# Performance work log

Measured on AMD Instinct MI355X. Metric: run time of the kernel, lower is better.

## Reference

```python
import jax, jax.numpy as jnp
import numpy as np

FP8_MAX = 448.0   # max normal of float8_e4m3fn
BLOCK = 128       # block_size
EPS = 1e-12


def setup_inputs() -> dict:
    key = jax.random.key(0)
    k1, k2 = jax.random.split(key)
    M, K, N = 8192, 2048, 2048  # tokens, in_features, out_features
    x = jax.random.normal(k1, (M, K), dtype=jnp.float32)
    # Build an fp8 blockwise-quantized weight (as the module stores it):
    w = jax.random.normal(k2, (N, K), dtype=jnp.float32) * 0.02
    wb = w.reshape(N // BLOCK, BLOCK, K // BLOCK, BLOCK)
    amax = jnp.max(jnp.abs(wb), axis=(1, 3))                      # [Nb, Kb]
    w_scale = jnp.maximum(amax, EPS) / FP8_MAX                    # fp32 per-block scale
    w_q = (wb / w_scale[:, None, :, None]).astype(jnp.float8_e4m3fn)
    weight = w_q.reshape(N, K)                                    # fp8 [N, K]
    return {"x": x, "weight": weight, "w_scale": w_scale}


def reference(x, weight, w_scale):
    M, K = x.shape
    N = weight.shape[0]
    # --- fp8_blockwise_act_quant: per (1, BLOCK) block along last dim ---
    xb = x.reshape(M, K // BLOCK, BLOCK)
    amax = jnp.max(jnp.abs(xb), axis=-1)                          # [M, Kb]
    x_scale = jnp.maximum(amax, EPS) / FP8_MAX                    # [M, Kb]
    x_q = (xb / x_scale[:, :, None]).astype(jnp.float8_e4m3fn).astype(jnp.float32)
    # --- blockwise_fp8_gemm: y[m,n] = sum_kb (xq_blk . wq_blk) * xs[m,kb] * ws[nb,kb]
    # Scales factor per-block, so dequantize then a single GEMM is exactly equivalent.
    x_deq = (x_q * x_scale[:, :, None]).reshape(M, K)             # [M, K]
    ws_full = jnp.repeat(jnp.repeat(w_scale, BLOCK, axis=0), BLOCK, axis=1)  # [N, K]
    w_deq = weight.astype(jnp.float32) * ws_full                  # [N, K]
    y = x_deq @ w_deq.T                                           # [M, N]
    return y
```

## Files before the change

### kernel.cpp

```cpp
#include <hip/hip_runtime.h>
#include <cstdint>
#include <cstddef>

#define MDIM 8192
#define KDIM 2048
#define NDIM 2048
#define QBLK 128
#define KB   (KDIM / QBLK)
#define NB   (NDIM / QBLK)

typedef float floatx4 __attribute__((ext_vector_type(4)));
typedef int   int4v   __attribute__((ext_vector_type(4)));
typedef int   int8v   __attribute__((ext_vector_type(8)));

#define AS1 __attribute__((address_space(1)))
#define AS3 __attribute__((address_space(3)))

__device__ inline float e4m3_rne(float q) {
    float aq = fabsf(q);
    float r;
    if (aq < 0.015625f) {
        r = rintf(aq * 512.0f) * 0.001953125f;
    } else {
        unsigned u = __float_as_uint(aq);
        unsigned rem = u & 0xFFFFFu;
        unsigned base = u & ~0xFFFFFu;
        unsigned inc = (rem > 0x80000u || (rem == 0x80000u && (u & 0x100000u))) ? 0x100000u : 0u;
        r = __uint_as_float(base + inc);
    }
    return q < 0.0f ? -r : r;
}

__device__ inline unsigned e4m3_encode(float r) {
    unsigned u = __float_as_uint(r);
    unsigned s = (u >> 24) & 0x80u;
    float a = fabsf(r);
    if (a < 0.015625f) return s | (unsigned)(a * 512.0f + 0.25f);
    unsigned e = ((u >> 23) & 0xFFu) - 120u;
    unsigned m = (u >> 20) & 7u;
    return s | (e << 3) | m;
}

__device__ inline float e4m3_decode(unsigned b) {
    unsigned s = b >> 7, e = (b >> 3) & 0xFu, m = b & 7u;
    float v;
    if (e == 0) v = (float)m * 0.001953125f;
    else        v = __uint_as_float((e + 120u) << 23) * (float)(8 + m) * 0.125f;
    return s ? -v : v;
}

__device__ inline int is_expbyte(unsigned b) {
    unsigned e = b & 0x7Fu;
    return (e >= 0x3Bu && e <= 0x43u) || e == 0x00u;
}

#define XQ_OFF  0
#define WQ_OFF  ((size_t)MDIM * KDIM)
#define XS_OFF  (WQ_OFF + (size_t)NDIM * KDIM)
#define FL_OFF  (XS_OFF + (size_t)MDIM * KB * 4)

#define QXB ((MDIM * KB) / 8)
#define DWB ((NDIM * KDIM / 8) / 256)

__global__ __launch_bounds__(256) void prep_kernel(const float* __restrict__ x,
                                                   const void* __restrict__ wq,
                                                   unsigned char* __restrict__ xq,
                                                   unsigned char* __restrict__ wq8,
                                                   float* __restrict__ xs,
                                                   int* __restrict__ flag) {
    const int tid = threadIdx.x;
    if (blockIdx.x == 0 && tid == 0) *flag = 0;

    if (blockIdx.x < QXB) {
        const int g = tid >> 5;
        const int l = tid & 31;
        const size_t bi = (size_t)blockIdx.x * 8 + g;
        const size_t base = bi << 7;

        const float4 v = *(const float4*)(x + base + (size_t)l * 4);
        float a = fmaxf(fmaxf(fabsf(v.x), fabsf(v.y)), fmaxf(fabsf(v.z), fabsf(v.w)));
        a = fmaxf(a, __shfl_xor(a, 1));
        a = fmaxf(a, __shfl_xor(a, 2));
        a = fmaxf(a, __shfl_xor(a, 4));
        a = fmaxf(a, __shfl_xor(a, 8));
        a = fmaxf(a, __shfl_xor(a, 16));

        const float scale = fmaxf(a, 1e-12f) / 448.0f;
        if (l == 0) xs[bi] = scale;

        unsigned b0 = e4m3_encode(e4m3_rne(v.x / scale));
        unsigned b1 = e4m3_encode(e4m3_rne(v.y / scale));
        unsigned b2 = e4m3_encode(e4m3_rne(v.z / scale));
        unsigned b3 = e4m3_encode(e4m3_rne(v.w / scale));
        *(unsigned*)(xq + base + (size_t)l * 4) = b0 | (b1 << 8) | (b2 << 16) | (b3 << 24);
    } else {
        const int lane = tid & 63;
        const unsigned pw = ((const unsigned*)wq)[lane];
        const unsigned long long m3 = __ballot(is_expbyte((pw >> 24) & 0xFFu));
        const unsigned long long m1 = __ballot(((pw >> 8) & 0xFFu) == 0u);
        const int f = (__popcll(m3) >= 56) ? ((__popcll(m1) >= 56) ? 2 : 1) : 0;

        const size_t idx = (size_t)(blockIdx.x - QXB) * 256 + tid;
        const size_t off = idx * 8;

        unsigned lo, hi;
        if (f == 2) {
            const float4* p = (const float4*)((const float*)wq + off);
            const float4 a = p[0], b = p[1];
            lo = e4m3_encode(a.x) | (e4m3_encode(a.y) << 8) | (e4m3_encode(a.z) << 16) | (e4m3_encode(a.w) << 24);
            hi = e4m3_encode(b.x) | (e4m3_encode(b.y) << 8) | (e4m3_encode(b.z) << 16) | (e4m3_encode(b.w) << 24);
        } else if (f == 1) {
            const ushort4 h0 = *(const ushort4*)((const unsigned short*)wq + off);
            const ushort4 h1 = *(((const ushort4*)((const unsigned short*)wq + off)) + 1);
            lo = e4m3_encode(__uint_as_float((unsigned)h0.x << 16))
               | (e4m3_encode(__uint_as_float((unsigned)h0.y << 16)) << 8)
               | (e4m3_encode(__uint_as_float((unsigned)h0.z << 16)) << 16)
               | (e4m3_encode(__uint_as_float((unsigned)h0.w << 16)) << 24);
            hi = e4m3_encode(__uint_as_float((unsigned)h1.x << 16))
               | (e4m3_encode(__uint_as_float((unsigned)h1.y << 16)) << 8)
               | (e4m3_encode(__uint_as_float((unsigned)h1.z << 16)) << 16)
               | (e4m3_encode(__uint_as_float((unsigned)h1.w << 16)) << 24);
        } else {
            const uint2 d = *(const uint2*)((const unsigned char*)wq + off);
            lo = d.x; hi = d.y;
        }
        *(uint2*)(wq8 + off) = make_uint2(lo, hi);
    }
}

__global__ __launch_bounds__(256, 2) void gemm_mx_kernel(const unsigned char* __restrict__ Aq,
                                                         const unsigned char* __restrict__ Bq,
                                                         const float* __restrict__ xs,
                                                         const float* __restrict__ wsc,
                                                         float* __restrict__ C) {
    __shared__ unsigned char sA[128 * 128];
    __shared__ unsigned char sB[128 * 128];

    const int tid  = threadIdx.x;
    const int wave = tid >> 6;
    const int lane = tid & 63;
    const int lrow = lane & 15;
    const int lk   = lane >> 4;
    const int wm   = (wave & 1) * 64;
    const int wn   = (wave >> 1) * 64;
    const int m0   = blockIdx.y * 128;
    const int n0   = blockIdx.x * 128;
    const int nb   = n0 >> 7;

    const int srow = tid >> 3;
    const int gck  = (tid & 7) ^ (srow & 7);
    const unsigned char* agp = Aq + (size_t)(m0 + srow) * KDIM + gck * 16;
    const unsigned char* bgp = Bq + (size_t)(n0 + srow) * KDIM + gck * 16;

    floatx4 acc[4][4] = {};
    const floatx4 zero = {0.f, 0.f, 0.f, 0.f};

    for (int kb = 0; kb < KB; ++kb) {
        const size_t koff = (size_t)kb * QBLK;
        __syncthreads();
#pragma unroll
        for (int it = 0; it < 4; ++it)
            __builtin_amdgcn_global_load_lds(
                (const AS1 void*)(agp + (size_t)(it * 32) * KDIM + koff),
                (AS3 void*)(sA + tid * 16 + it * 4096), 16, 0, 0);
#pragma unroll
        for (int it = 0; it < 4; ++it)
            __builtin_amdgcn_global_load_lds(
                (const AS1 void*)(bgp + (size_t)(it * 32) * KDIM + koff),
                (AS3 void*)(sB + tid * 16 + it * 4096), 16, 0, 0);
        __syncthreads();

        int8v af[4], bf[4];
#pragma unroll
        for (int i = 0; i < 4; ++i) {
            const int Ra = wm + i * 16 + lrow;
            const int c0 = (lk * 2) ^ (Ra & 7);
            const int c1 = (lk * 2 + 1) ^ (Ra & 7);
            int4v alo = *(const int4v*)(sA + Ra * 128 + c0 * 16);
            int4v ahi = *(const int4v*)(sA + Ra * 128 + c1 * 16);
            af[i] = __builtin_shufflevector(alo, ahi, 0, 1, 2, 3, 4, 5, 6, 7);
            const int Rb = wn + i * 16 + lrow;
            const int d0 = (lk * 2) ^ (Rb & 7);
            const int d1 = (lk * 2 + 1) ^ (Rb & 7);
            int4v blo = *(const int4v*)(sB + Rb * 128 + d0 * 16);
            int4v bhi = *(const int4v*)(sB + Rb * 128 + d1 * 16);
            bf[i] = __builtin_shufflevector(blo, bhi, 0, 1, 2, 3, 4, 5, 6, 7);
        }

        const float wsk = wsc[nb * KB + kb];
        float cs[4][4];
#pragma unroll
        for (int i = 0; i < 4; ++i)
#pragma unroll
            for (int r = 0; r < 4; ++r)
                cs[i][r] = xs[(size_t)(m0 + wm + i * 16 + lk * 4 + r) * KB + kb] * wsk;

#pragma unroll
        for (int i = 0; i < 4; ++i)
#pragma unroll
            for (int j = 0; j < 4; ++j) {
                floatx4 blk = __builtin_amdgcn_mfma_scale_f32_16x16x128_f8f6f4(
                    af[i], bf[j], zero, 0, 0, 0, 0x7F7F7F7F, 0, 0x7F7F7F7F);
#pragma unroll
                for (int r = 0; r < 4; ++r)
                    acc[i][j][r] += cs[i][r] * blk[r];
            }
    }

#pragma unroll
    for (int i = 0; i < 4; ++i) {
        const int row0 = m0 + wm + i * 16 + lk * 4;
#pragma unroll
        for (int r = 0; r < 4; ++r) {
            float* cp = C + (size_t)(row0 + r) * NDIM + n0 + wn + lrow;
#pragma unroll
            for (int j = 0; j < 4; ++j)
                cp[j * 16] = acc[i][j][r];
        }
    }
}

__global__ __launch_bounds__(256) void check_kernel(const unsigned char* __restrict__ xq,
                                                    const unsigned char* __restrict__ wq8,
                                                    const float* __restrict__ xs,
                                                    const float* __restrict__ wsc,
                                                    const float* __restrict__ y,
                                                    int* __restrict__ flag) {
    const int s = blockIdx.x;
    const int m = (s * 1237 + 11) & (MDIM - 1);
    const int n = (s * 389 + 7) & (NDIM - 1);
    const int tid = threadIdx.x;
    const int k0 = tid * 8;
    const int kb = k0 >> 7;

    const unsigned char* xp = xq + (size_t)m * KDIM + k0;
    const unsigned char* wp = wq8 + (size_t)n * KDIM + k0;
    float dot = 0.f;
#pragma unroll
    for (int i = 0; i < 8; ++i)
        dot += e4m3_decode(xp[i]) * e4m3_decode(wp[i]);
    float part = dot * xs[m * KB + kb] * wsc[(n >> 7) * KB + kb];

#pragma unroll
    for (int o = 32; o > 0; o >>= 1) part += __shfl_down(part, o);
    __shared__ float wsum[4];
    if ((tid & 63) == 0) wsum[tid >> 6] = part;
    __syncthreads();
    if (tid == 0) {
        const float tot = wsum[0] + wsum[1] + wsum[2] + wsum[3];
        const float d = tot - y[(size_t)m * NDIM + n];
        if (!(fabsf(d) <= 0.05f)) atomicOr(flag, 1);
    }
}

__global__ __launch_bounds__(256, 2) void gemm_fb_kernel(const unsigned char* __restrict__ Aq,
                                                         const unsigned char* __restrict__ Bq,
                                                         const float* __restrict__ xs,
                                                         const float* __restrict__ wsc,
                                                         float* __restrict__ C,
                                                         const int* __restrict__ flag) {
    if (*flag == 0) return;

    __shared__ unsigned char sA[128 * 128];
    __shared__ unsigned char sB[128 * 128];

    const int tid  = threadIdx.x;
    const int wave = tid >> 6;
    const int lane = tid & 63;
    const int lrow = lane & 15;
    const int lk   = lane >> 4;
    const int wm   = (wave & 1) * 64;
    const int wn   = (wave >> 1) * 64;
    const int m0   = blockIdx.y * 128;
    const int n0   = blockIdx.x * 128;
    const int nb   = n0 >> 7;

    const int srow = tid >> 3;
    const int gck  = (tid & 7) ^ (srow & 7);
    const unsigned char* agp = Aq + (size_t)(m0 + srow) * KDIM + gck * 16;
    const unsigned char* bgp = Bq + (size_t)(n0 + srow) * KDIM + gck * 16;

    floatx4 acc[4][4] = {};

    for (int kb = 0; kb < KB; ++kb) {
        const size_t koff = (size_t)kb * QBLK;
        __syncthreads();
#pragma unroll
        for (int it = 0; it < 4; ++it)
            __builtin_amdgcn_global_load_lds(
                (const AS1 void*)(agp + (size_t)(it * 32) * KDIM + koff),
                (AS3 void*)(sA + tid * 16 + it * 4096), 16, 0, 0);
#pragma unroll
        for (int it = 0; it < 4; ++it)
            __builtin_amdgcn_global_load_lds(
                (const AS1 void*)(bgp + (size_t)(it * 32) * KDIM + koff),
                (AS3 void*)(sB + tid * 16 + it * 4096), 16, 0, 0);
        __syncthreads();

        floatx4 blk[4][4] = {};
#pragma unroll
        for (int ks = 0; ks < 4; ++ks) {
            long a8[4], b8[4];
            const int lc = ks * 2 + (lk >> 1);
            const int bo = (lk & 1) * 8;
#pragma unroll
            for (int i = 0; i < 4; ++i) {
                const int Ra = wm + i * 16 + lrow;
                a8[i] = *(const long*)(sA + Ra * 128 + (lc ^ (Ra & 7)) * 16 + bo);
                const int Rb = wn + i * 16 + lrow;
                b8[i] = *(const long*)(sB + Rb * 128 + (lc ^ (Rb & 7)) * 16 + bo);
            }
#pragma unroll
            for (int i = 0; i < 4; ++i)
#pragma unroll
                for (int j = 0; j < 4; ++j)
                    blk[i][j] = __builtin_amdgcn_mfma_f32_16x16x32_fp8_fp8(a8[i], b8[j], blk[i][j], 0, 0, 0);
        }

        const float wsk = wsc[nb * KB + kb];
#pragma unroll
        for (int i = 0; i < 4; ++i) {
            float cs[4];
#pragma unroll
            for (int r = 0; r < 4; ++r)
                cs[r] = xs[(size_t)(m0 + wm + i * 16 + lk * 4 + r) * KB + kb] * wsk;
#pragma unroll
            for (int j = 0; j < 4; ++j)
#pragma unroll
                for (int r = 0; r < 4; ++r)
                    acc[i][j][r] += cs[r] * blk[i][j][r];
        }
    }

#pragma unroll
    for (int i = 0; i < 4; ++i) {
        const int row0 = m0 + wm + i * 16 + lk * 4;
#pragma unroll
        for (int r = 0; r < 4; ++r) {
            float* cp = C + (size_t)(row0 + r) * NDIM + n0 + wn + lrow;
#pragma unroll
            for (int j = 0; j < 4; ++j)
                cp[j * 16] = acc[i][j][r];
        }
    }
}

extern "C" void kernel_launch(void* const* d_in, const int* in_sizes, int n_in,
                              void* d_out, int out_size, void* d_ws, size_t ws_size,
                              hipStream_t stream) {
    const float* x      = (const float*)d_in[0];
    const void* wq      = d_in[1];
    const float* wscale = (const float*)d_in[2];
    float* y            = (float*)d_out;

    unsigned char* xq  = (unsigned char*)d_ws + XQ_OFF;
    unsigned char* wq8 = (unsigned char*)d_ws + WQ_OFF;
    float* xs          = (float*)((unsigned char*)d_ws + XS_OFF);
    int* flag          = (int*)((unsigned char*)d_ws + FL_OFF);

    prep_kernel<<<QXB + DWB, 256, 0, stream>>>(x, wq, xq, wq8, xs, flag);
    gemm_mx_kernel<<<dim3(NDIM / 128, MDIM / 128), 256, 0, stream>>>(xq, wq8, xs, wscale, y);
    check_kernel<<<64, 256, 0, stream>>>(xq, wq8, xs, wscale, y, flag);
    gemm_fb_kernel<<<dim3(NDIM / 128, MDIM / 128), 256, 0, stream>>>(xq, wq8, xs, wscale, y, flag);
}
```

Before: 184.0 us.

## Enlarge GEMM tile to 256x256 with LDS double buffering and hardware fp8 conversion

The GEMM moves from 128x128 tiles with 256 threads to 256x256 tiles with 512 threads, and each wave now computes a 128x64 sub-tile. The kernel double-buffers the A/B LDS stages so the next k-block loads while the current one computes, stages the activation scales in shared memory, and remaps block IDs so neighbouring blocks share tiles in cache. Separately, the activation quantization swaps the software e4m3 rounding and encoding for the packed cvt_pk_fp8_f32 hardware instruction. The larger tile doubles the per-thread accumulator registers and uses about 144KB of LDS, which may limit occupancy, and the hardware conversion could handle saturation or rounding differently from the software path.

```diff
diff --git a/kernel.cpp b/kernel.cpp
--- a/kernel.cpp
+++ b/kernel.cpp
@@ -88,11 +88,11 @@
         const float scale = fmaxf(a, 1e-12f) / 448.0f;
         if (l == 0) xs[bi] = scale;
 
-        unsigned b0 = e4m3_encode(e4m3_rne(v.x / scale));
-        unsigned b1 = e4m3_encode(e4m3_rne(v.y / scale));
-        unsigned b2 = e4m3_encode(e4m3_rne(v.z / scale));
-        unsigned b3 = e4m3_encode(e4m3_rne(v.w / scale));
-        *(unsigned*)(xq + base + (size_t)l * 4) = b0 | (b1 << 8) | (b2 << 16) | (b3 << 24);
+        const float q0 = v.x / scale, q1 = v.y / scale;
+        const float q2 = v.z / scale, q3 = v.w / scale;
+        int w = __builtin_amdgcn_cvt_pk_fp8_f32(q0, q1, 0, false);
+        w = __builtin_amdgcn_cvt_pk_fp8_f32(q2, q3, w, true);
+        *(unsigned*)(xq + base + (size_t)l * 4) = (unsigned)w;
     } else {
         const int lane = tid & 63;
         const unsigned pw = ((const unsigned*)wq)[lane];
@@ -128,91 +128,114 @@
     }
 }
 
-__global__ __launch_bounds__(256, 2) void gemm_mx_kernel(const unsigned char* __restrict__ Aq,
+__global__ __launch_bounds__(512, 2) void gemm_mx_kernel(const unsigned char* __restrict__ Aq,
                                                          const unsigned char* __restrict__ Bq,
                                                          const float* __restrict__ xs,
                                                          const float* __restrict__ wsc,
                                                          float* __restrict__ C) {
-    __shared__ unsigned char sA[128 * 128];
-    __shared__ unsigned char sB[128 * 128];
+    __shared__ unsigned char sA[2][256 * 128];
+    __shared__ unsigned char sB[2][256 * 128];
+    __shared__ float sxs[KB][256];
 
     const int tid  = threadIdx.x;
     const int wave = tid >> 6;
     const int lane = tid & 63;
     const int lrow = lane & 15;
     const int lk   = lane >> 4;
-    const int wm   = (wave & 1) * 64;
-    const int wn   = (wave >> 1) * 64;
-    const int m0   = blockIdx.y * 128;
-    const int n0   = blockIdx.x * 128;
-    const int nb   = n0 >> 7;
+    const int wml  = (wave >> 2) * 128;
+    const int wnl  = (wave & 3) * 64;
+
+    const int bid = blockIdx.x;
+    const int lid = ((bid & 7) << 5) + (bid >> 3);
+    const int m0  = (lid >> 3) * 256;
+    const int n0  = (lid & 7) * 256;
+    const int nb  = (n0 + wnl) >> 7;
 
     const int srow = tid >> 3;
     const int gck  = (tid & 7) ^ (srow & 7);
     const unsigned char* agp = Aq + (size_t)(m0 + srow) * KDIM + gck * 16;
     const unsigned char* bgp = Bq + (size_t)(n0 + srow) * KDIM + gck * 16;
 
-    floatx4 acc[4][4] = {};
+#define STAGE(buf, kb_) do {                                                          \
+    const size_t koff_ = (size_t)(kb_) * QBLK;                                        \
+    _Pragma("unroll")                                                                 \
+    for (int it = 0; it < 4; ++it)                                                    \
+        __builtin_amdgcn_global_load_lds(                                             \
+            (const AS1 void*)(agp + (size_t)(it * 64) * KDIM + koff_),                \
+            (AS3 void*)(&sA[buf][0] + tid * 16 + it * 8192), 16, 0, 0);               \
+    _Pragma("unroll")                                                                 \
+    for (int it = 0; it < 4; ++it)                                                    \
+        __builtin_amdgcn_global_load_lds(                                             \
+            (const AS1 void*)(bgp + (size_t)(it * 64) * KDIM + koff_),                \
+            (AS3 void*)(&sB[buf][0] + tid * 16 + it * 8192), 16, 0, 0);               \
+} while (0)
+
+    STAGE(0, 0);
+    if (tid < 256) {
+        const float4* xp = (const float4*)(xs + (size_t)(m0 + tid) * KB);
+#pragma unroll
+        for (int q = 0; q < 4; ++q) {
+            const float4 v = xp[q];
+            sxs[q * 4 + 0][tid] = v.x;
+            sxs[q * 4 + 1][tid] = v.y;
+            sxs[q * 4 + 2][tid] = v.z;
+            sxs[q * 4 + 3][tid] = v.w;
+        }
+    }
+    __syncthreads();
+
+    floatx4 acc[8][4] = {};
     const floatx4 zero = {0.f, 0.f, 0.f, 0.f};
 
     for (int kb = 0; kb < KB; ++kb) {
-        const size_t koff = (size_t)kb * QBLK;
-        __syncthreads();
-#pragma unroll
-        for (int it = 0; it < 4; ++it)
-            __builtin_amdgcn_global_load_lds(
-                (const AS1 void*)(agp + (size_t)(it * 32) * KDIM + koff),
-                (AS3 void*)(sA + tid * 16 + it * 4096), 16, 0, 0);
-#pragma unroll
-        for (int it = 0; it < 4; ++it)
-            __builtin_amdgcn_global_load_lds(
-                (const AS1 void*)(bgp + (size_t)(it * 32) * KDIM + koff),
-                (AS3 void*)(sB + tid * 16 + it * 4096), 16, 0, 0);
-        __syncthreads();
-
-        int8v af[4], bf[4];
-#pragma unroll
-        for (int i = 0; i < 4; ++i) {
-            const int Ra = wm + i * 16 + lrow;
+        const int cur = kb & 1;
+        if (kb + 1 < KB) STAGE(cur ^ 1, kb + 1);
+
+        int8v bf[4];
+#pragma unroll
+        for (int j = 0; j < 4; ++j) {
+            const int Rb = wnl + j * 16 + lrow;
+            const int d0 = (lk * 2) ^ (Rb & 7);
+            const int d1 = (lk * 2 + 1) ^ (Rb & 7);
+            int4v blo = *(const int4v*)(&sB[cur][0] + Rb * 128 + d0 * 16);
+            int4v bhi = *(const int4v*)(&sB[cur][0] + Rb * 128 + d1 * 16);
+            bf[j] = __builtin_shufflevector(blo, bhi, 0, 1, 2, 3, 4, 5, 6, 7);
+        }
+        const float wsk = wsc[nb * KB + kb];
+
+#pragma unroll
+        for (int i = 0; i < 8; ++i) {
+            const int Ra = wml + i * 16 + lrow;
             const int c0 = (lk * 2) ^ (Ra & 7);
             const int c1 = (lk * 2 + 1) ^ (Ra & 7);
-            int4v alo = *(const int4v*)(sA + Ra * 128 + c0 * 16);
-            int4v ahi = *(const int4v*)(sA + Ra * 128 + c1 * 16);
-            af[i] = __builtin_shufflevector(alo, ahi, 0, 1, 2, 3, 4, 5, 6, 7);
-            const int Rb = wn + i * 16 + lrow;
-            const int d0 = (lk * 2) ^ (Rb & 7);
-            const int d1 = (lk * 2 + 1) ^ (Rb & 7);
-            int4v blo = *(const int4v*)(sB + Rb * 128 + d0 * 16);
-            int4v bhi = *(const int4v*)(sB + Rb * 128 + d1 * 16);
-            bf[i] = __builtin_shufflevector(blo, bhi, 0, 1, 2, 3, 4, 5, 6, 7);
-        }
-
-        const float wsk = wsc[nb * KB + kb];
-        float cs[4][4];
-#pragma unroll
-        for (int i = 0; i < 4; ++i)
-#pragma unroll
-            for (int r = 0; r < 4; ++r)
-                cs[i][r] = xs[(size_t)(m0 + wm + i * 16 + lk * 4 + r) * KB + kb] * wsk;
-
-#pragma unroll
-        for (int i = 0; i < 4; ++i)
+            int4v alo = *(const int4v*)(&sA[cur][0] + Ra * 128 + c0 * 16);
+            int4v ahi = *(const int4v*)(&sA[cur][0] + Ra * 128 + c1 * 16);
+            int8v af = __builtin_shufflevector(alo, ahi, 0, 1, 2, 3, 4, 5, 6, 7);
+
+            const float4 xv = *(const float4*)(&sxs[kb][wml + i * 16 + lk * 4]);
+            const float cs0 = xv.x * wsk, cs1 = xv.y * wsk;
+            const float cs2 = xv.z * wsk, cs3 = xv.w * wsk;
+
 #pragma unroll
             for (int j = 0; j < 4; ++j) {
                 floatx4 blk = __builtin_amdgcn_mfma_scale_f32_16x16x128_f8f6f4(
-                    af[i], bf[j], zero, 0, 0, 0, 0x7F7F7F7F, 0, 0x7F7F7F7F);
-#pragma unroll
-                for (int r = 0; r < 4; ++r)
-                    acc[i][j][r] += cs[i][r] * blk[r];
+                    af, bf[j], zero, 0, 0, 0, 0x7F7F7F7F, 0, 0x7F7F7F7F);
+                acc[i][j][0] += cs0 * blk[0];
+                acc[i][j][1] += cs1 * blk[1];
+                acc[i][j][2] += cs2 * blk[2];
+                acc[i][j][3] += cs3 * blk[3];
             }
-    }
-
-#pragma unroll
-    for (int i = 0; i < 4; ++i) {
-        const int row0 = m0 + wm + i * 16 + lk * 4;
+        }
+        __syncthreads();
+    }
+#undef STAGE
+
+#pragma unroll
+    for (int i = 0; i < 8; ++i) {
+        const int row0 = m0 + wml + i * 16 + lk * 4;
 #pragma unroll
         for (int r = 0; r < 4; ++r) {
-            float* cp = C + (size_t)(row0 + r) * NDIM + n0 + wn + lrow;
+            float* cp = C + (size_t)(row0 + r) * NDIM + n0 + wnl + lrow;
 #pragma unroll
             for (int j = 0; j < 4; ++j)
                 cp[j * 16] = acc[i][j][r];
@@ -359,7 +382,7 @@
     int* flag          = (int*)((unsigned char*)d_ws + FL_OFF);
 
     prep_kernel<<<QXB + DWB, 256, 0, stream>>>(x, wq, xq, wq8, xs, flag);
-    gemm_mx_kernel<<<dim3(NDIM / 128, MDIM / 128), 256, 0, stream>>>(xq, wq8, xs, wscale, y);
+    gemm_mx_kernel<<<(MDIM / 256) * (NDIM / 256), 512, 0, stream>>>(xq, wq8, xs, wscale, y);
     check_kernel<<<64, 256, 0, stream>>>(xq, wq8, xs, wscale, y, flag);
     gemm_fb_kernel<<<dim3(NDIM / 128, MDIM / 128), 256, 0, stream>>>(xq, wq8, xs, wscale, y, flag);
 }
```

Result: faster. 174.1 us (-5.4%).

## Double-buffer GEMM LDS tiles, cache scales in LDS, swizzle blocks, restructure prep

Applied to the files above, without the earlier changes.

The GEMM kernel now double-buffers the A/B tiles in LDS, issuing the next k-block's async global-to-LDS loads before computing the current one, with one barrier per iteration. Activation and weight scales are preloaded into shared memory, scaling is vectorised, and the 1D grid is remapped to group blocks for better L2 reuse. The prep kernel becomes a fixed-size grid-stride kernel, has each thread handle eight elements, and uses hardware fp8 pack-convert instructions instead of software rounding. This doubles LDS use, which may lower occupancy. The hardware conversion's rounding and saturation may differ from the software encoder.

```diff
diff --git a/kernel.cpp b/kernel.cpp
--- a/kernel.cpp
+++ b/kernel.cpp
@@ -59,8 +59,9 @@
 #define XS_OFF  (WQ_OFF + (size_t)NDIM * KDIM)
 #define FL_OFF  (XS_OFF + (size_t)MDIM * KB * 4)
 
-#define QXB ((MDIM * KB) / 8)
+#define QXB ((MDIM * KB) / 16)
 #define DWB ((NDIM * KDIM / 8) / 256)
+#define PREP_GRID 2048
 
 __global__ __launch_bounds__(256) void prep_kernel(const float* __restrict__ x,
                                                    const void* __restrict__ wq,
@@ -71,36 +72,41 @@
     const int tid = threadIdx.x;
     if (blockIdx.x == 0 && tid == 0) *flag = 0;
 
-    if (blockIdx.x < QXB) {
-        const int g = tid >> 5;
-        const int l = tid & 31;
-        const size_t bi = (size_t)blockIdx.x * 8 + g;
+    const int g = tid >> 4;
+    const int l = tid & 15;
+    for (int blk = blockIdx.x; blk < QXB; blk += PREP_GRID) {
+        const size_t bi = (size_t)blk * 16 + g;
         const size_t base = bi << 7;
 
-        const float4 v = *(const float4*)(x + base + (size_t)l * 4);
-        float a = fmaxf(fmaxf(fabsf(v.x), fabsf(v.y)), fmaxf(fabsf(v.z), fabsf(v.w)));
+        const float4* xp = (const float4*)(x + base + (size_t)l * 8);
+        const float4 v0 = xp[0], v1 = xp[1];
+        float a = fmaxf(fmaxf(fmaxf(fabsf(v0.x), fabsf(v0.y)), fmaxf(fabsf(v0.z), fabsf(v0.w))),
+                        fmaxf(fmaxf(fabsf(v1.x), fabsf(v1.y)), fmaxf(fabsf(v1.z), fabsf(v1.w))));
         a = fmaxf(a, __shfl_xor(a, 1));
         a = fmaxf(a, __shfl_xor(a, 2));
         a = fmaxf(a, __shfl_xor(a, 4));
         a = fmaxf(a, __shfl_xor(a, 8));
-        a = fmaxf(a, __shfl_xor(a, 16));
 
         const float scale = fmaxf(a, 1e-12f) / 448.0f;
         if (l == 0) xs[bi] = scale;
 
-        unsigned b0 = e4m3_encode(e4m3_rne(v.x / scale));
-        unsigned b1 = e4m3_encode(e4m3_rne(v.y / scale));
-        unsigned b2 = e4m3_encode(e4m3_rne(v.z / scale));
-        unsigned b3 = e4m3_encode(e4m3_rne(v.w / scale));
-        *(unsigned*)(xq + base + (size_t)l * 4) = b0 | (b1 << 8) | (b2 << 16) | (b3 << 24);
-    } else {
-        const int lane = tid & 63;
-        const unsigned pw = ((const unsigned*)wq)[lane];
-        const unsigned long long m3 = __ballot(is_expbyte((pw >> 24) & 0xFFu));
-        const unsigned long long m1 = __ballot(((pw >> 8) & 0xFFu) == 0u);
-        const int f = (__popcll(m3) >= 56) ? ((__popcll(m1) >= 56) ? 2 : 1) : 0;
-
-        const size_t idx = (size_t)(blockIdx.x - QXB) * 256 + tid;
+        const float q0 = v0.x / scale, q1 = v0.y / scale, q2 = v0.z / scale, q3 = v0.w / scale;
+        const float q4 = v1.x / scale, q5 = v1.y / scale, q6 = v1.z / scale, q7 = v1.w / scale;
+        int w0 = __builtin_amdgcn_cvt_pk_fp8_f32(q0, q1, 0, false);
+        w0 = __builtin_amdgcn_cvt_pk_fp8_f32(q2, q3, w0, true);
+        int w1 = __builtin_amdgcn_cvt_pk_fp8_f32(q4, q5, 0, false);
+        w1 = __builtin_amdgcn_cvt_pk_fp8_f32(q6, q7, w1, true);
+        *(uint2*)(xq + base + (size_t)l * 8) = make_uint2((unsigned)w0, (unsigned)w1);
+    }
+
+    const int lane = tid & 63;
+    const unsigned pw = ((const unsigned*)wq)[lane];
+    const unsigned long long m3 = __ballot(is_expbyte((pw >> 24) & 0xFFu));
+    const unsigned long long m1 = __ballot(((pw >> 8) & 0xFFu) == 0u);
+    const int f = (__popcll(m3) >= 56) ? ((__popcll(m1) >= 56) ? 2 : 1) : 0;
+
+    for (int blk = blockIdx.x; blk < DWB; blk += PREP_GRID) {
+        const size_t idx = (size_t)blk * 256 + tid;
         const size_t off = idx * 8;
 
         unsigned lo, hi;
@@ -133,67 +139,87 @@
                                                          const float* __restrict__ xs,
                                                          const float* __restrict__ wsc,
                                                          float* __restrict__ C) {
-    __shared__ unsigned char sA[128 * 128];
-    __shared__ unsigned char sB[128 * 128];
+    __shared__ unsigned char sA[2][128 * 128];
+    __shared__ unsigned char sB[2][128 * 128];
+    __shared__ float sxs[KB][128];
+    __shared__ float swk[KB];
 
     const int tid  = threadIdx.x;
     const int wave = tid >> 6;
     const int lane = tid & 63;
     const int lrow = lane & 15;
     const int lk   = lane >> 4;
+    const int lk4  = lk * 4;
     const int wm   = (wave & 1) * 64;
     const int wn   = (wave >> 1) * 64;
-    const int m0   = blockIdx.y * 128;
-    const int n0   = blockIdx.x * 128;
-    const int nb   = n0 >> 7;
+
+    const int bid = blockIdx.x;
+    const int lid = ((bid & 7) << 7) | (bid >> 3);
+    const int m0  = (lid >> 4) * 128;
+    const int n0  = (lid & 15) * 128;
+    const int nb  = n0 >> 7;
 
     const int srow = tid >> 3;
     const int gck  = (tid & 7) ^ (srow & 7);
-    const unsigned char* agp = Aq + (size_t)(m0 + srow) * KDIM + gck * 16;
-    const unsigned char* bgp = Bq + (size_t)(n0 + srow) * KDIM + gck * 16;
+    const unsigned char* agp = Aq + (size_t)(m0 + srow) * KDIM + (size_t)gck * 16;
+    const unsigned char* bgp = Bq + (size_t)(n0 + srow) * KDIM + (size_t)gck * 16;
+
+#define GL(SRC, DST) __builtin_amdgcn_global_load_lds((const AS1 void*)(SRC), (AS3 void*)(DST), 16, 0, 0)
+#define STAGE(buf, kb_) do {                                                          \
+    const size_t koff_ = (size_t)(kb_) * QBLK;                                        \
+    _Pragma("unroll")                                                                 \
+    for (int it = 0; it < 4; ++it)                                                    \
+        GL(agp + (size_t)(it * 32) * KDIM + koff_, &sA[buf][0] + tid * 16 + it * 4096); \
+    _Pragma("unroll")                                                                 \
+    for (int it = 0; it < 4; ++it)                                                    \
+        GL(bgp + (size_t)(it * 32) * KDIM + koff_, &sB[buf][0] + tid * 16 + it * 4096); \
+} while (0)
+
+    STAGE(0, 0);
+    if (tid < 128) {
+        const float4* xp = (const float4*)(xs + (size_t)(m0 + tid) * KB);
+#pragma unroll
+        for (int q = 0; q < 4; ++q) {
+            const float4 v = xp[q];
+            sxs[q * 4 + 0][tid] = v.x;
+            sxs[q * 4 + 1][tid] = v.y;
+            sxs[q * 4 + 2][tid] = v.z;
+            sxs[q * 4 + 3][tid] = v.w;
+        }
+    }
+    if (tid < KB) swk[tid] = wsc[nb * KB + tid];
+    __syncthreads();
 
     floatx4 acc[4][4] = {};
     const floatx4 zero = {0.f, 0.f, 0.f, 0.f};
 
-    for (int kb = 0; kb < KB; ++kb) {
-        const size_t koff = (size_t)kb * QBLK;
-        __syncthreads();
-#pragma unroll
-        for (int it = 0; it < 4; ++it)
-            __builtin_amdgcn_global_load_lds(
-                (const AS1 void*)(agp + (size_t)(it * 32) * KDIM + koff),
-                (AS3 void*)(sA + tid * 16 + it * 4096), 16, 0, 0);
-#pragma unroll
-        for (int it = 0; it < 4; ++it)
-            __builtin_amdgcn_global_load_lds(
-                (const AS1 void*)(bgp + (size_t)(it * 32) * KDIM + koff),
-                (AS3 void*)(sB + tid * 16 + it * 4096), 16, 0, 0);
-        __syncthreads();
+#define FRAG(dst, basep, ROW) do {                                              \
+    const int _r = (ROW);                                                       \
+    const unsigned char* _p = (basep) + _r * 128;                               \
+    const int _c0 = (lk * 2) ^ (_r & 7);                                        \
+    ((int4v*)&(dst))[0] = *(const int4v*)(_p + _c0 * 16);                       \
+    ((int4v*)&(dst))[1] = *(const int4v*)(_p + (_c0 ^ 1) * 16);                 \
+} while (0)
+
+    for (int t = 0; t < KB; ++t) {
+        const int cur = t & 1;
+        const unsigned char* sAc = &sA[cur][0];
+        const unsigned char* sBc = &sB[cur][0];
+
+        if (t + 1 < KB) STAGE(cur ^ 1, t + 1);
 
         int8v af[4], bf[4];
 #pragma unroll
         for (int i = 0; i < 4; ++i) {
-            const int Ra = wm + i * 16 + lrow;
-            const int c0 = (lk * 2) ^ (Ra & 7);
-            const int c1 = (lk * 2 + 1) ^ (Ra & 7);
-            int4v alo = *(const int4v*)(sA + Ra * 128 + c0 * 16);
-            int4v ahi = *(const int4v*)(sA + Ra * 128 + c1 * 16);
-            af[i] = __builtin_shufflevector(alo, ahi, 0, 1, 2, 3, 4, 5, 6, 7);
-            const int Rb = wn + i * 16 + lrow;
-            const int d0 = (lk * 2) ^ (Rb & 7);
-            const int d1 = (lk * 2 + 1) ^ (Rb & 7);
-            int4v blo = *(const int4v*)(sB + Rb * 128 + d0 * 16);
-            int4v bhi = *(const int4v*)(sB + Rb * 128 + d1 * 16);
-            bf[i] = __builtin_shufflevector(blo, bhi, 0, 1, 2, 3, 4, 5, 6, 7);
-        }
-
-        const float wsk = wsc[nb * KB + kb];
-        float cs[4][4];
+            FRAG(af[i], sAc, wm + i * 16 + lrow);
+            FRAG(bf[i], sBc, wn + i * 16 + lrow);
+        }
+
+        const float wsk = swk[t];
+        floatx4 cs[4];
 #pragma unroll
         for (int i = 0; i < 4; ++i)
-#pragma unroll
-            for (int r = 0; r < 4; ++r)
-                cs[i][r] = xs[(size_t)(m0 + wm + i * 16 + lk * 4 + r) * KB + kb] * wsk;
+            cs[i] = (*(const floatx4*)&sxs[t][wm + i * 16 + lk4]) * wsk;
 
 #pragma unroll
         for (int i = 0; i < 4; ++i)
@@ -201,15 +227,18 @@
             for (int j = 0; j < 4; ++j) {
                 floatx4 blk = __builtin_amdgcn_mfma_scale_f32_16x16x128_f8f6f4(
                     af[i], bf[j], zero, 0, 0, 0, 0x7F7F7F7F, 0, 0x7F7F7F7F);
-#pragma unroll
-                for (int r = 0; r < 4; ++r)
-                    acc[i][j][r] += cs[i][r] * blk[r];
+                acc[i][j] += cs[i] * blk;
             }
-    }
+
+        __syncthreads();
+    }
+#undef FRAG
+#undef STAGE
+#undef GL
 
 #pragma unroll
     for (int i = 0; i < 4; ++i) {
-        const int row0 = m0 + wm + i * 16 + lk * 4;
+        const int row0 = m0 + wm + i * 16 + lk4;
 #pragma unroll
         for (int r = 0; r < 4; ++r) {
             float* cp = C + (size_t)(row0 + r) * NDIM + n0 + wn + lrow;
@@ -358,8 +387,8 @@
     float* xs          = (float*)((unsigned char*)d_ws + XS_OFF);
     int* flag          = (int*)((unsigned char*)d_ws + FL_OFF);
 
-    prep_kernel<<<QXB + DWB, 256, 0, stream>>>(x, wq, xq, wq8, xs, flag);
-    gemm_mx_kernel<<<dim3(NDIM / 128, MDIM / 128), 256, 0, stream>>>(xq, wq8, xs, wscale, y);
+    prep_kernel<<<PREP_GRID, 256, 0, stream>>>(x, wq, xq, wq8, xs, flag);
+    gemm_mx_kernel<<<(MDIM / 128) * (NDIM / 128), 256, 0, stream>>>(xq, wq8, xs, wscale, y);
     check_kernel<<<64, 256, 0, stream>>>(xq, wq8, xs, wscale, y, flag);
     gemm_fb_kernel<<<dim3(NDIM / 128, MDIM / 128), 256, 0, stream>>>(xq, wq8, xs, wscale, y, flag);
 }
```

Measured after the change: 681.6 us. 3.7x slower.
